# Kernel tuning notes

Hardware: AMD Instinct MI355X
Metric: run time of the kernel (lower is better)

The kernel has to match this reference:

```python
import jax, jax.numpy as jnp
import numpy as np

jax.config.update('jax_enable_x64', True)  # 60-bit packed voxel ids need int64

V, H, W, C, P = 8, 128, 128, 512, 128
VOXEL_SIZE = 0.05
NUM_VOXELS = 120000  # target_num_voxels; upper bound on unique voxels here
MAXI = (1 << 20) - 1


def _layernorm(x, g, b, eps=1e-5):
    mu = jnp.mean(x, axis=-1, keepdims=True)
    var = jnp.mean((x - mu) ** 2, axis=-1, keepdims=True)
    return (x - mu) * jax.lax.rsqrt(var + eps) * g + b


def setup_inputs() -> dict:
    key = jax.random.key(0)
    ks = jax.random.split(key, 16)
    features = jax.random.normal(ks[0], (V, H, W, C), jnp.float32)
    depth = jax.random.uniform(ks[1], (V, H, W), jnp.float32, minval=0.2, maxval=1.0)
    K = jnp.broadcast_to(jnp.array([[100.0, 0.0, W / 2.0], [0.0, 100.0, H / 2.0], [0.0, 0.0, 1.0]], jnp.float32), (V, 3, 3))
    R = jnp.broadcast_to(jnp.eye(3, dtype=jnp.float32), (V, 3, 3))
    t = jax.random.uniform(ks[2], (V, 3, 1), jnp.float32, minval=-0.1, maxval=0.1)
    extrinsics = jnp.concatenate([R, t], axis=-1)  # [V,3,4] world->cam
    conf = jax.random.normal(ks[3], (V, H, W), jnp.float32)
    s = 0.02
    return {
        'features': features, 'depth': depth, 'intrinsics': K, 'extrinsics': extrinsics, 'conf': conf,
        'w_proj1': jax.random.normal(ks[4], (C, C), jnp.float32) * s, 'b_proj1': jnp.zeros((C,), jnp.float32),
        'g_ln1': jnp.ones((C,), jnp.float32), 'be_ln1': jnp.zeros((C,), jnp.float32),
        'w_proj2': jax.random.normal(ks[5], (C, C), jnp.float32) * s, 'b_proj2': jnp.zeros((C,), jnp.float32),
        'w_pos1': jax.random.normal(ks[6], (3, P), jnp.float32) * s, 'b_pos1': jnp.zeros((P,), jnp.float32),
        'w_pos2': jax.random.normal(ks[7], (P, P), jnp.float32) * s, 'b_pos2': jnp.zeros((P,), jnp.float32),
        'w_fuse': jax.random.normal(ks[8], (C + P, C), jnp.float32) * s, 'b_fuse': jnp.zeros((C,), jnp.float32),
        'g_ln2': jnp.ones((C,), jnp.float32), 'be_ln2': jnp.zeros((C,), jnp.float32),
    }


def reference(features, depth, intrinsics, extrinsics, conf,
              w_proj1, b_proj1, g_ln1, be_ln1, w_proj2, b_proj2,
              w_pos1, b_pos1, w_pos2, b_pos2, w_fuse, b_fuse, g_ln2, be_ln2):
    # ---- backproject depth to world coords ----
    y, x = jnp.meshgrid(jnp.arange(H, dtype=depth.dtype), jnp.arange(W, dtype=depth.dtype), indexing='ij')
    pixels = jnp.stack([x, y, jnp.ones_like(x)], axis=-1).reshape(H * W, 3)  # [HW,3]
    Kinv = jnp.linalg.inv(intrinsics)                                        # [V,3,3]
    cam = jnp.einsum('vij,pj->vpi', Kinv, pixels) * depth.reshape(V, H * W, 1)
    cam_h = jnp.concatenate([cam, jnp.ones((V, H * W, 1), cam.dtype)], axis=-1)
    bottom = jnp.broadcast_to(jnp.array([[0.0, 0.0, 0.0, 1.0]], extrinsics.dtype), (V, 1, 4))
    E4 = jnp.concatenate([extrinsics, bottom], axis=1)                       # world->cam 4x4
    Einv = jnp.linalg.inv(E4)                                                # cam->world
    world = jnp.einsum('vij,vpj->vpi', Einv[:, :3, :], cam_h)                # [V,HW,3]
    pts = world.reshape(-1, 3)                                               # [N,3]

    # ---- voxel indices + packed 60-bit voxel id ----
    vox = pts / VOXEL_SIZE
    idx = jnp.round(vox).astype(jnp.int64)
    ix = jnp.clip(idx[:, 0], 0, MAXI)
    iy = jnp.clip(idx[:, 1], 0, MAXI)
    iz = jnp.clip(idx[:, 2], 0, MAXI)
    vid = (ix << 40) | (iy << 20) | iz                                       # [N]

    # ---- group points by voxel id (static-size unique -> segment ids) ----
    u_ids, seg = jnp.unique(vid, size=NUM_VOXELS, fill_value=-1, return_inverse=True)
    seg = seg.reshape(-1)

    # ---- per-voxel softmax pooling weights (scatter_max + scatter_add) ----
    scores = jax.nn.softplus(conf.reshape(-1))
    m = jax.ops.segment_max(scores, seg, num_segments=NUM_VOXELS)
    e = jnp.exp(scores - m[seg])
    denom = jax.ops.segment_sum(e, seg, num_segments=NUM_VOXELS)
    wgt = e / jnp.maximum(denom[seg], 1e-12)

    # ---- weighted scatter-add of features ----
    feats = features.reshape(-1, C)
    vfeat = jax.ops.segment_sum(feats * wgt[:, None], seg, num_segments=NUM_VOXELS)  # [S,C]

    # ---- voxel centers decoded from packed id ----
    cxi = (u_ids >> 40) & MAXI
    cyi = (u_ids >> 20) & MAXI
    czi = u_ids & MAXI
    valid = (u_ids >= 0)
    centers = jnp.stack([cxi, cyi, czi], axis=-1).astype(vfeat.dtype) * VOXEL_SIZE
    centers = jnp.where(valid[:, None], centers, 0.0)

    # ---- voxel_feat_proj: Linear -> LN -> GELU -> Linear ----
    h = vfeat @ w_proj1 + b_proj1
    h = jax.nn.gelu(_layernorm(h, g_ln1, be_ln1), approximate=False)
    h = h @ w_proj2 + b_proj2

    # ---- pos_encoding: Linear -> SiLU -> Linear ----
    pe = jax.nn.silu(centers @ w_pos1 + b_pos1) @ w_pos2 + b_pos2

    # ---- token_fusion: Linear -> LN -> GELU ----
    tok = jnp.concatenate([h, pe], axis=-1) @ w_fuse + b_fuse
    tok = jax.nn.gelu(_layernorm(tok, g_ln2, be_ln2), approximate=False)
    return tok * valid[:, None].astype(tok.dtype)
```

## Files before the change

kernel.cpp:

```cpp
#include <hip/hip_runtime.h>
#include <hip/hip_bf16.h>
#include <math.h>

#define V 8
#define H 128
#define W 128
#define C 512
#define P 128
#define HW (H*W)
#define NPTS (V*HW)
#define MAXI ((1<<20)-1)
#define ROWCAP 8192
#define NROWS 120000
#define DGRID 65536
#define PERM(d) ((((d) & 15) << 12) | ((d) >> 4))

#define SCAT_BLOCKS 512
#define WT_BLOCKS   832
#define POS_BLOCKS  (ROWCAP/8)
#define ZERO_BLOCKS 512
#define MEGA_BLOCKS (SCAT_BLOCKS + WT_BLOCKS + POS_BLOCKS + ZERO_BLOCKS)

typedef __attribute__((ext_vector_type(8))) short short8v;
typedef __attribute__((ext_vector_type(4))) float f32x4;

__device__ __forceinline__ float softplusf(float x){
  return fmaxf(x, 0.0f) + log1pf(expf(-fabsf(x)));
}
__device__ __forceinline__ float geluf(float x){
  return 0.5f * x * (1.0f + erff(x * 0.70710678118654752440f));
}
__device__ __forceinline__ short f2bf_s(float x){
  __hip_bfloat16 h = __float2bfloat16(x);
  return *(short*)&h;
}

__device__ void wT_tile(const float* __restrict__ w, __hip_bfloat16* __restrict__ wT,
                        int K, int bx, int by){
  __shared__ float tile[32][33];
  int kb = bx*32, nb = by*32;
  int tx = threadIdx.x & 31, ty = threadIdx.x >> 5;
  for (int i = ty; i < 32; i += 8){
    int k = kb + i;
    tile[i][tx] = (k < K) ? w[(size_t)k*512 + nb + tx] : 0.f;
  }
  __syncthreads();
  for (int i = ty; i < 32; i += 8){
    int n = nb + i;
    int k = kb + tx;
    if (k < K) wT[(size_t)n*K + k] = __float2bfloat16(tile[tx][i]);
  }
}

__global__ __launch_bounds__(256) void k_points(const float* __restrict__ depth,
    const float* __restrict__ Kmat, const float* __restrict__ Emat,
    int* __restrict__ scnt, unsigned short* __restrict__ didp, int* __restrict__ witp){
  int p = blockIdx.x*256 + threadIdx.x;
  int v = blockIdx.x >> 6;
  const float* K = Kmat + v*9;
  float a=K[0],b=K[1],c=K[2],d=K[3],e=K[4],f=K[5],g=K[6],h=K[7],i=K[8];
  float det = a*(e*i-f*h) - b*(d*i-f*g) + c*(d*h-e*g);
  float kin = 1.0f/det;
  float k0=(e*i-f*h)*kin, k1=(c*h-b*i)*kin, k2=(b*f-c*e)*kin;
  float k3=(f*g-d*i)*kin, k4=(a*i-c*g)*kin, k5=(c*d-a*f)*kin;
  float k6=(d*h-e*g)*kin, k7=(b*g-a*h)*kin, k8=(a*e-b*d)*kin;
  const float* E = Emat + v*12;
  float r00=E[0],r01=E[1],r02=E[2],t0=E[3];
  float r10=E[4],r11=E[5],r12=E[6],t1=E[7];
  float r20=E[8],r21=E[9],r22=E[10],t2=E[11];
  float rdet = r00*(r11*r22-r12*r21) - r01*(r10*r22-r12*r20) + r02*(r10*r21-r11*r20);
  float rinv = 1.0f/rdet;
  float i00=(r11*r22-r12*r21)*rinv, i01=(r02*r21-r01*r22)*rinv, i02=(r01*r12-r02*r11)*rinv;
  float i10=(r12*r20-r10*r22)*rinv, i11=(r00*r22-r02*r20)*rinv, i12=(r02*r10-r00*r12)*rinv;
  float i20=(r10*r21-r11*r20)*rinv, i21=(r01*r20-r00*r21)*rinv, i22=(r00*r11-r01*r10)*rinv;
  float j0=-(i00*t0+i01*t1+i02*t2), j1=-(i10*t0+i11*t1+i12*t2), j2=-(i20*t0+i21*t1+i22*t2);

  int pix = p & (HW-1);
  float fx = (float)(pix & 127);
  float fy = (float)(pix >> 7);
  float dep = depth[p];
  float cx = (k0*fx + k1*fy + k2) * dep;
  float cy = (k3*fx + k4*fy + k5) * dep;
  float cz = (k6*fx + k7*fy + k8) * dep;
  float wx = i00*cx + i01*cy + i02*cz + j0;
  float wy = i10*cx + i11*cy + i12*cz + j1;
  float wz = i20*cx + i21*cy + i22*cz + j2;
  long long ix = (long long)rintf(wx / 0.05f);
  long long iy = (long long)rintf(wy / 0.05f);
  long long iz = (long long)rintf(wz / 0.05f);
  ix = ix < 0 ? 0 : (ix > MAXI ? (long long)MAXI : ix);
  iy = iy < 0 ? 0 : (iy > MAXI ? (long long)MAXI : iy);
  iz = iz < 0 ? 0 : (iz > MAXI ? (long long)MAXI : iz);
  int dx = (int)(ix > 31 ? 31 : ix);
  int dy = (int)(iy > 31 ? 31 : iy);
  int dz = (int)(iz > 63 ? 63 : iz);
  int did = (dx << 11) | (dy << 6) | dz;
  didp[p] = (unsigned short)did;
  witp[p] = atomicAdd(&scnt[PERM(did)], 1);
}

__global__ __launch_bounds__(256) void k_scan1(const int* __restrict__ scnt,
    int* __restrict__ exwb, int* __restrict__ bsum){
  int tid = threadIdx.x;
  int did = blockIdx.x*256 + tid;
  int cnt = scnt[PERM(did)];
  int vpk = (cnt << 13) | (cnt > 0);
  int lane = tid & 63, wv = tid >> 6;
  int s = vpk;
  #pragma unroll
  for (int off = 1; off < 64; off <<= 1){
    int t = __shfl_up(s, off);
    if (lane >= off) s += t;
  }
  __shared__ int wsum[4];
  if (lane == 63) wsum[wv] = s;
  __syncthreads();
  int woff = 0;
  #pragma unroll
  for (int k = 0; k < 4; k++) woff += (k < wv) ? wsum[k] : 0;
  int incl = s + woff;
  exwb[did] = incl - vpk;
  if (tid == 255) bsum[blockIdx.x] = incl;
}

__global__ __launch_bounds__(256) void k_scan2(const int* __restrict__ scnt,
    const int* __restrict__ exwb, const int* __restrict__ bsum,
    int* __restrict__ row_of_dense, int* __restrict__ ustart_dense,
    int* __restrict__ dense_of_row, int* __restrict__ Sc){
  int tid = threadIdx.x, b = blockIdx.x;
  int lane = tid & 63, wv = tid >> 6;
  int vsum = (tid < b) ? bsum[tid] : 0;
  #pragma unroll
  for (int off = 32; off; off >>= 1) vsum += __shfl_down(vsum, off);
  __shared__ int rsum[4];
  if (lane == 0) rsum[wv] = vsum;
  __syncthreads();
  int prefix = rsum[0] + rsum[1] + rsum[2] + rsum[3];
  int did = b*256 + tid;
  int cnt = scnt[PERM(did)];
  int excl = exwb[did] + prefix;
  ustart_dense[did] = excl >> 13;
  int row = excl & 8191;
  row_of_dense[did] = row;
  if (cnt > 0) dense_of_row[row] = did;
  if (b == 255 && tid == 255)
    *Sc = (excl + ((cnt << 13) | (cnt > 0))) & 8191;
}

__global__ __launch_bounds__(256) void k_fill(const unsigned short* __restrict__ didp,
    const int* __restrict__ witp, const int* __restrict__ row_of_dense,
    const int* __restrict__ ustart_dense, const float* __restrict__ conf,
    int* __restrict__ pcsr, int* __restrict__ rcsr, float* __restrict__ wcsr){
  int p = blockIdx.x*256 + threadIdx.x;
  int did = didp[p];
  int idx = ustart_dense[did] + witp[p];
  pcsr[idx] = p;
  rcsr[idx] = row_of_dense[did];
  wcsr[idx] = expf(softplusf(conf[p]));
}

__global__ __launch_bounds__(256) void k_mega(
    const float* __restrict__ feats,
    const int* __restrict__ pcsr, const int* __restrict__ rcsr, const float* __restrict__ wcsr,
    float* __restrict__ vraw, float* __restrict__ esum,
    float* __restrict__ outp, const int* __restrict__ Sc,
    const int* __restrict__ dense_of_row,
    const float* __restrict__ wp1, const float* __restrict__ bp1,
    const float* __restrict__ wp2, const float* __restrict__ bp2,
    __hip_bfloat16* __restrict__ pebf,
    const float* __restrict__ w1, __hip_bfloat16* __restrict__ w1T,
    const float* __restrict__ w2, __hip_bfloat16* __restrict__ w2T,
    const float* __restrict__ wf, __hip_bfloat16* __restrict__ wfT){
  int blk = blockIdx.x;
  int tid = threadIdx.x;

  if (blk < SCAT_BLOCKS){
    __shared__ int pp[4][64];
    __shared__ int rr[4][64];
    __shared__ float ww[4][64];
    int q = tid >> 6, ln = tid & 63;
    int e = blk*256 + q*64 + ln;
    pp[q][ln] = pcsr[e];
    rr[q][ln] = rcsr[e];
    ww[q][ln] = wcsr[e];
    __syncthreads();
    f32x4 acc0 = (f32x4){0.f,0.f,0.f,0.f};
    f32x4 acc1 = (f32x4){0.f,0.f,0.f,0.f};
    float acce = 0.f;
    int cur = rr[q][0];
    #define FLUSH_ROW() { \
      float* vp = &vraw[(size_t)cur*C + ln*4]; \
      atomicAdd(vp+0, acc0[0]); atomicAdd(vp+1, acc0[1]); \
      atomicAdd(vp+2, acc0[2]); atomicAdd(vp+3, acc0[3]); \
      float* vq = vp + 256; \
      atomicAdd(vq+0, acc1[0]); atomicAdd(vq+1, acc1[1]); \
      atomicAdd(vq+2, acc1[2]); atomicAdd(vq+3, acc1[3]); \
      if (ln == 0) atomicAdd(&esum[cur], acce); \
      acc0 = (f32x4){0.f,0.f,0.f,0.f}; acc1 = (f32x4){0.f,0.f,0.f,0.f}; acce = 0.f; }
    for (int i = 0; i < 64; i += 4){
      int p0 = pp[q][i+0], p1 = pp[q][i+1], p2 = pp[q][i+2], p3 = pp[q][i+3];
      const float* f0 = feats + (size_t)p0*C + ln*4;
      const float* f1 = feats + (size_t)p1*C + ln*4;
      const float* f2 = feats + (size_t)p2*C + ln*4;
      const float* f3 = feats + (size_t)p3*C + ln*4;
      f32x4 a0 = *(const f32x4*)f0, b0 = *(const f32x4*)(f0 + 256);
      f32x4 a1 = *(const f32x4*)f1, b1 = *(const f32x4*)(f1 + 256);
      f32x4 a2 = *(const f32x4*)f2, b2 = *(const f32x4*)(f2 + 256);
      f32x4 a3 = *(const f32x4*)f3, b3 = *(const f32x4*)(f3 + 256);
      int r0 = rr[q][i+0], r1 = rr[q][i+1], r2 = rr[q][i+2], r3 = rr[q][i+3];
      float w0 = ww[q][i+0], w1_ = ww[q][i+1], w2_ = ww[q][i+2], w3 = ww[q][i+3];
      if (r0 != cur){ FLUSH_ROW(); cur = r0; }
      acc0 += a0 * w0; acc1 += b0 * w0; acce += w0;
      if (r1 != cur){ FLUSH_ROW(); cur = r1; }
      acc0 += a1 * w1_; acc1 += b1 * w1_; acce += w1_;
      if (r2 != cur){ FLUSH_ROW(); cur = r2; }
      acc0 += a2 * w2_; acc1 += b2 * w2_; acce += w2_;
      if (r3 != cur){ FLUSH_ROW(); cur = r3; }
      acc0 += a3 * w3; acc1 += b3 * w3; acce += w3;
    }
    FLUSH_ROW();
    #undef FLUSH_ROW
    return;
  }
  blk -= SCAT_BLOCKS;

  if (blk < WT_BLOCKS){
    if (blk < 256)      wT_tile(w1, w1T, 512, blk & 15, blk >> 4);
    else if (blk < 512){ int t = blk - 256; wT_tile(w2, w2T, 512, t & 15, t >> 4); }
    else               { int t = blk - 512; wT_tile(wf, wfT, 640, t % 20, t / 20); }
    return;
  }
  blk -= WT_BLOCKS;

  if (blk < POS_BLOCKS){
    int S = *Sc; if (S > ROWCAP) S = ROWCAP;
    int r0 = blk * 8;
    if (r0 >= S) return;
    __shared__ float t1[8][128];
    __shared__ float cen[8][4];
    if (tid < 8){
      int r = r0 + tid;
      int d = (r < S) ? dense_of_row[r] : 0;
      cen[tid][0] = (float)(d >> 11) * 0.05f;
      cen[tid][1] = (float)((d >> 6) & 31) * 0.05f;
      cen[tid][2] = (float)(d & 63) * 0.05f;
    }
    __syncthreads();
    #pragma unroll
    for (int it = 0; it < 4; it++){
      int idx = tid + it*256;
      int r = idx >> 7, j = idx & 127;
      float a = cen[r][0]*wp1[j] + cen[r][1]*wp1[P + j] + cen[r][2]*wp1[2*P + j] + bp1[j];
      t1[r][j] = a / (1.0f + expf(-a));
    }
    __syncthreads();
    #pragma unroll
    for (int it = 0; it < 4; it++){
      int idx = tid + it*256;
      int r = idx >> 7, j = idx & 127;
      if (r0 + r < S){
        float acc = bp2[j];
        for (int k = 0; k < P; k++) acc = fmaf(t1[r][k], wp2[k*P + j], acc);
        pebf[(size_t)(r0+r)*P + j] = __float2bfloat16(acc);
      }
    }
    return;
  }
  blk -= POS_BLOCKS;

  {
    int S = *Sc; if (S > ROWCAP) S = ROWCAP;
    f32x4* out4 = (f32x4*)outp;
    size_t start = (size_t)S * 128;
    size_t total = (size_t)NROWS * 128;
    size_t stride = (size_t)ZERO_BLOCKS * 256;
    f32x4 z = (f32x4){0.f,0.f,0.f,0.f};
    for (size_t idx = start + (size_t)blk*256 + tid; idx < total; idx += stride)
      __builtin_nontemporal_store(z, &out4[idx]);
  }
}

__global__ __launch_bounds__(256) void k_gemm1(const float* __restrict__ vraw,
    const float* __restrict__ esum, const __hip_bfloat16* __restrict__ Bt,
    const float* __restrict__ bias, float* __restrict__ Cout, const int* __restrict__ Sc){
  int S = *Sc; if (S > ROWCAP) S = ROWCAP;
  int m0 = blockIdx.y * 64;
  if (m0 >= S) return;
  int n0 = blockIdx.x * 64;
  __shared__ short As[64][40];
  __shared__ short Bs[64][40];
  int tid = threadIdx.x;
  int l = tid & 63, w = tid >> 6;
  int wr = w >> 1, wc = w & 1;
  f32x4 acc[2][2];
  #pragma unroll
  for (int i=0;i<2;i++)
    #pragma unroll
    for (int j=0;j<2;j++) acc[i][j] = (f32x4){0.f,0.f,0.f,0.f};

  int arow = tid >> 2, akq = tid & 3;
  int gm = m0 + arow;
  float inv = 0.f;
  if (gm < S) inv = 1.0f / fmaxf(esum[gm], 1e-12f);
  for (int kb = 0; kb < 512; kb += 32){
    {
      int kg = kb + akq*8;
      short8v av = (short8v){0,0,0,0,0,0,0,0};
      if (gm < S){
        f32x4 va = *(const f32x4*)(vraw + (size_t)gm*512 + kg);
        f32x4 vb = *(const f32x4*)(vraw + (size_t)gm*512 + kg + 4);
        av[0]=f2bf_s(va[0]*inv); av[1]=f2bf_s(va[1]*inv);
        av[2]=f2bf_s(va[2]*inv); av[3]=f2bf_s(va[3]*inv);
        av[4]=f2bf_s(vb[0]*inv); av[5]=f2bf_s(vb[1]*inv);
        av[6]=f2bf_s(vb[2]*inv); av[7]=f2bf_s(vb[3]*inv);
      }
      *(short8v*)&As[arow][akq*8] = av;
      short8v bv = *(const short8v*)(Bt + (size_t)(n0 + arow)*512 + kb + akq*8);
      *(short8v*)&Bs[arow][akq*8] = bv;
    }
    __syncthreads();
    short8v a0 = *(const short8v*)&As[wr*32 + (l & 15)][(l >> 4)*8];
    short8v a1 = *(const short8v*)&As[wr*32 + 16 + (l & 15)][(l >> 4)*8];
    short8v b0 = *(const short8v*)&Bs[wc*32 + (l & 15)][(l >> 4)*8];
    short8v b1 = *(const short8v*)&Bs[wc*32 + 16 + (l & 15)][(l >> 4)*8];
    acc[0][0] = __builtin_amdgcn_mfma_f32_16x16x32_bf16(a0, b0, acc[0][0], 0, 0, 0);
    acc[0][1] = __builtin_amdgcn_mfma_f32_16x16x32_bf16(a0, b1, acc[0][1], 0, 0, 0);
    acc[1][0] = __builtin_amdgcn_mfma_f32_16x16x32_bf16(a1, b0, acc[1][0], 0, 0, 0);
    acc[1][1] = __builtin_amdgcn_mfma_f32_16x16x32_bf16(a1, b1, acc[1][1], 0, 0, 0);
    __syncthreads();
  }
  float bias0 = bias[n0 + wc*32 +  0 + (l & 15)];
  float bias1 = bias[n0 + wc*32 + 16 + (l & 15)];
  #pragma unroll
  for (int i = 0; i < 2; i++){
    #pragma unroll
    for (int j = 0; j < 2; j++){
      int n = n0 + wc*32 + j*16 + (l & 15);
      float bj = j ? bias1 : bias0;
      #pragma unroll
      for (int r = 0; r < 4; r++){
        int m = m0 + wr*32 + i*16 + (l >> 4)*4 + r;
        if (m < S) Cout[(size_t)m*512 + n] = acc[i][j][r] + bj;
      }
    }
  }
}

template<int OUTBF>
__global__ __launch_bounds__(256) void k_gemm_mfma(
    const __hip_bfloat16* __restrict__ A1, int lda1, int K1,
    const __hip_bfloat16* __restrict__ A2, int lda2,
    const __hip_bfloat16* __restrict__ Bt, int ldb,
    const float* __restrict__ bias, void* __restrict__ Cout,
    int Kdim, const int* __restrict__ Sc){
  int S = *Sc; if (S > ROWCAP) S = ROWCAP;
  int m0 = blockIdx.y * 64;
  if (m0 >= S) return;
  int n0 = blockIdx.x * 64;
  __shared__ short As[64][40];
  __shared__ short Bs[64][40];
  int tid = threadIdx.x;
  int l = tid & 63, w = tid >> 6;
  int wr = w >> 1, wc = w & 1;
  f32x4 acc[2][2];
  #pragma unroll
  for (int i=0;i<2;i++)
    #pragma unroll
    for (int j=0;j<2;j++) acc[i][j] = (f32x4){0.f,0.f,0.f,0.f};

  int arow = tid >> 2, akq = tid & 3;
  for (int kb = 0; kb < Kdim; kb += 32){
    {
      int kg = kb + akq*8;
      short8v av = (short8v){0,0,0,0,0,0,0,0};
      int gm = m0 + arow;
      if (gm < S){
        const __hip_bfloat16* src = (kg < K1) ? (A1 + (size_t)gm*lda1 + kg)
                                              : (A2 + (size_t)gm*lda2 + (kg - K1));
        av = *(const short8v*)src;
      }
      *(short8v*)&As[arow][akq*8] = av;
      short8v bv = *(const short8v*)(Bt + (size_t)(n0 + arow)*ldb + kb + akq*8);
      *(short8v*)&Bs[arow][akq*8] = bv;
    }
    __syncthreads();
    short8v a0 = *(const short8v*)&As[wr*32 + (l & 15)][(l >> 4)*8];
    short8v a1 = *(const short8v*)&As[wr*32 + 16 + (l & 15)][(l >> 4)*8];
    short8v b0 = *(const short8v*)&Bs[wc*32 + (l & 15)][(l >> 4)*8];
    short8v b1 = *(const short8v*)&Bs[wc*32 + 16 + (l & 15)][(l >> 4)*8];
    acc[0][0] = __builtin_amdgcn_mfma_f32_16x16x32_bf16(a0, b0, acc[0][0], 0, 0, 0);
    acc[0][1] = __builtin_amdgcn_mfma_f32_16x16x32_bf16(a0, b1, acc[0][1], 0, 0, 0);
    acc[1][0] = __builtin_amdgcn_mfma_f32_16x16x32_bf16(a1, b0, acc[1][0], 0, 0, 0);
    acc[1][1] = __builtin_amdgcn_mfma_f32_16x16x32_bf16(a1, b1, acc[1][1], 0, 0, 0);
    __syncthreads();
  }
  float bias0 = bias[n0 + wc*32 +  0 + (l & 15)];
  float bias1 = bias[n0 + wc*32 + 16 + (l & 15)];
  #pragma unroll
  for (int i = 0; i < 2; i++){
    #pragma unroll
    for (int j = 0; j < 2; j++){
      int n = n0 + wc*32 + j*16 + (l & 15);
      float bj = j ? bias1 : bias0;
      #pragma unroll
      for (int r = 0; r < 4; r++){
        int m = m0 + wr*32 + i*16 + (l >> 4)*4 + r;
        if (m < S){
          float val = acc[i][j][r] + bj;
          if (OUTBF) ((__hip_bfloat16*)Cout)[(size_t)m*512 + n] = __float2bfloat16(val);
          else       ((float*)Cout)[(size_t)m*512 + n] = val;
        }
      }
    }
  }
}

__global__ __launch_bounds__(256) void k_ln_gelu(const float* __restrict__ in,
    __hip_bfloat16* __restrict__ outp, const float* __restrict__ g, const float* __restrict__ b,
    const int* __restrict__ Sc){
  int S = *Sc; if (S > ROWCAP) S = ROWCAP;
  __shared__ float red[8];
  int lane = threadIdx.x & 63, wid = threadIdx.x >> 6;
  for (int row = blockIdx.x; row < S; row += gridDim.x){
    float x0 = in[(size_t)row*C + threadIdx.x];
    float x1 = in[(size_t)row*C + threadIdx.x + 256];
    float s = x0 + x1;
    for (int o_=32;o_;o_>>=1) s += __shfl_down(s, o_);
    if (lane == 0) red[wid] = s;
    __syncthreads();
    float mu = (red[0]+red[1]+red[2]+red[3]) * (1.0f/C);
    __syncthreads();
    float d0 = x0-mu, d1 = x1-mu;
    float q = d0*d0 + d1*d1;
    for (int o_=32;o_;o_>>=1) q += __shfl_down(q, o_);
    if (lane == 0) red[wid] = q;
    __syncthreads();
    float var = (red[0]+red[1]+red[2]+red[3]) * (1.0f/C);
    float rs = rsqrtf(var + 1e-5f);
    float y0 = d0*rs*g[threadIdx.x]     + b[threadIdx.x];
    float y1 = d1*rs*g[threadIdx.x+256] + b[threadIdx.x+256];
    outp[(size_t)row*C + threadIdx.x]       = __float2bfloat16(geluf(y0));
    outp[(size_t)row*C + threadIdx.x + 256] = __float2bfloat16(geluf(y1));
    __syncthreads();
  }
}

__global__ __launch_bounds__(256) void k_ln_gelu_out(const float* __restrict__ in,
    float* __restrict__ outp, const float* __restrict__ g, const float* __restrict__ b,
    const int* __restrict__ Sc){
  int S = *Sc; if (S > ROWCAP) S = ROWCAP;
  __shared__ float red[8];
  int lane = threadIdx.x & 63, wid = threadIdx.x >> 6;
  for (int row = blockIdx.x; row < S; row += gridDim.x){
    float x0 = in[(size_t)row*C + threadIdx.x];
    float x1 = in[(size_t)row*C + threadIdx.x + 256];
    float s = x0 + x1;
    for (int o_=32;o_;o_>>=1) s += __shfl_down(s, o_);
    if (lane == 0) red[wid] = s;
    __syncthreads();
    float mu = (red[0]+red[1]+red[2]+red[3]) * (1.0f/C);
    __syncthreads();
    float d0 = x0-mu, d1 = x1-mu;
    float q = d0*d0 + d1*d1;
    for (int o_=32;o_;o_>>=1) q += __shfl_down(q, o_);
    if (lane == 0) red[wid] = q;
    __syncthreads();
    float var = (red[0]+red[1]+red[2]+red[3]) * (1.0f/C);
    float rs = rsqrtf(var + 1e-5f);
    float y0 = d0*rs*g[threadIdx.x]     + b[threadIdx.x];
    float y1 = d1*rs*g[threadIdx.x+256] + b[threadIdx.x+256];
    __builtin_nontemporal_store(geluf(y0), &outp[(size_t)row*C + threadIdx.x]);
    __builtin_nontemporal_store(geluf(y1), &outp[(size_t)row*C + threadIdx.x + 256]);
    __syncthreads();
  }
}

extern "C" void kernel_launch(void* const* d_in, const int* in_sizes, int n_in,
                              void* d_out, int out_size, void* d_ws, size_t ws_size,
                              hipStream_t stream){
  const float* features = (const float*)d_in[0];
  const float* depth    = (const float*)d_in[1];
  const float* intr     = (const float*)d_in[2];
  const float* extr     = (const float*)d_in[3];
  const float* conf     = (const float*)d_in[4];
  const float* w1  = (const float*)d_in[5];
  const float* b1  = (const float*)d_in[6];
  const float* g1  = (const float*)d_in[7];
  const float* be1 = (const float*)d_in[8];
  const float* w2  = (const float*)d_in[9];
  const float* b2  = (const float*)d_in[10];
  const float* wp1 = (const float*)d_in[11];
  const float* bp1 = (const float*)d_in[12];
  const float* wp2 = (const float*)d_in[13];
  const float* bp2 = (const float*)d_in[14];
  const float* wf  = (const float*)d_in[15];
  const float* bf  = (const float*)d_in[16];
  const float* g2  = (const float*)d_in[17];
  const float* be2 = (const float*)d_in[18];

  char* ws = (char*)d_ws;
  size_t o = 0;
  auto alloc = [&](size_t bytes){ void* p = ws + o; o += (bytes + 255) & ~size_t(255); return p; };
  int*   scnt    = (int*)alloc((size_t)DGRID*4);
  int*   Sc      = (int*)alloc(256);
  float* esum    = (float*)alloc((size_t)ROWCAP*4);
  float* vraw    = (float*)alloc((size_t)ROWCAP*C*4);
  size_t zspan = (size_t)((char*)vraw + (size_t)ROWCAP*C*4 - (char*)scnt);
  unsigned short* didp = (unsigned short*)alloc((size_t)NPTS*2);
  int*   witp    = (int*)alloc((size_t)NPTS*4);
  int*   pcsr    = (int*)alloc((size_t)NPTS*4);
  int*   rcsr    = (int*)alloc((size_t)NPTS*4);
  float* wcsr    = (float*)alloc((size_t)NPTS*4);
  int*   exwb    = (int*)alloc((size_t)DGRID*4);
  int*   bsum    = (int*)alloc(256*4);
  int*   row_of_dense   = (int*)alloc((size_t)DGRID*4);
  int*   ustart_dense   = (int*)alloc((size_t)DGRID*4);
  int*   dense_of_row   = (int*)alloc((size_t)ROWCAP*4);
  float*          hbufA = (float*)alloc((size_t)ROWCAP*C*4);
  __hip_bfloat16* h1bf = (__hip_bfloat16*)alloc((size_t)ROWCAP*C*2);
  __hip_bfloat16* h2bf = (__hip_bfloat16*)alloc((size_t)ROWCAP*C*2);
  __hip_bfloat16* pebf = (__hip_bfloat16*)alloc((size_t)ROWCAP*P*2);
  __hip_bfloat16* w1T  = (__hip_bfloat16*)alloc((size_t)512*512*2);
  __hip_bfloat16* w2T  = (__hip_bfloat16*)alloc((size_t)512*512*2);
  __hip_bfloat16* wfT  = (__hip_bfloat16*)alloc((size_t)512*640*2);

  float* outp = (float*)d_out;

  hipMemsetAsync(scnt, 0, zspan, stream);

  k_points<<<NPTS/256, 256, 0, stream>>>(depth, intr, extr, scnt, didp, witp);
  k_scan1<<<DGRID/256, 256, 0, stream>>>(scnt, exwb, bsum);
  k_scan2<<<DGRID/256, 256, 0, stream>>>(scnt, exwb, bsum, row_of_dense, ustart_dense,
                                         dense_of_row, Sc);
  k_fill<<<NPTS/256, 256, 0, stream>>>(didp, witp, row_of_dense, ustart_dense, conf,
                                       pcsr, rcsr, wcsr);
  k_mega<<<MEGA_BLOCKS, 256, 0, stream>>>(features, pcsr, rcsr, wcsr, vraw, esum,
                                          outp, Sc, dense_of_row,
                                          wp1, bp1, wp2, bp2, pebf,
                                          w1, w1T, w2, w2T, wf, wfT);

  dim3 gg(512/64, ROWCAP/64);
  k_gemm1<<<gg, 256, 0, stream>>>(vraw, esum, w1T, b1, hbufA, Sc);
  k_ln_gelu<<<2048, 256, 0, stream>>>(hbufA, h1bf, g1, be1, Sc);
  k_gemm_mfma<1><<<gg, 256, 0, stream>>>(h1bf, 512, 512, h1bf, 512, w2T, 512, b2, h2bf, 512, Sc);
  k_gemm_mfma<0><<<gg, 256, 0, stream>>>(h2bf, 512, 512, pebf, 128, wfT, 640, bf, hbufA, 640, Sc);
  k_ln_gelu_out<<<2048, 256, 0, stream>>>(hbufA, outp, g2, be2, Sc);
}
```

Baseline: 233.9 us.

## Spread output tail zero-fill across earlier kernels and widen scatter ILP

```diff
diff --git a/kernel.cpp b/kernel.cpp
--- a/kernel.cpp
+++ b/kernel.cpp
@@ -11,15 +11,19 @@
 #define NPTS (V*HW)
 #define MAXI ((1<<20)-1)
 #define ROWCAP 8192
+#define PROWCAP 5376
 #define NROWS 120000
 #define DGRID 65536
 #define PERM(d) ((((d) & 15) << 12) | ((d) >> 4))
-
-#define SCAT_BLOCKS 512
+#define NCH 5
+
+#define SCAT_BLOCKS 1024
 #define WT_BLOCKS   832
 #define POS_BLOCKS  (ROWCAP/8)
-#define ZERO_BLOCKS 512
-#define MEGA_BLOCKS (SCAT_BLOCKS + WT_BLOCKS + POS_BLOCKS + ZERO_BLOCKS)
+#define MEGA_BLOCKS (SCAT_BLOCKS + WT_BLOCKS + POS_BLOCKS)
+
+#define PZB 512
+#define GZB 512
 
 typedef __attribute__((ext_vector_type(8))) short short8v;
 typedef __attribute__((ext_vector_type(4))) float f32x4;
@@ -33,6 +37,21 @@
 __device__ __forceinline__ short f2bf_s(float x){
   __hip_bfloat16 h = __float2bfloat16(x);
   return *(short*)&h;
+}
+
+__device__ __forceinline__ void zero_chunk(float* __restrict__ outp, int chunk,
+                                           int nblocks, int blk, int tid){
+  f32x4* out4 = (f32x4*)outp;
+  size_t start = (size_t)PROWCAP * 128;
+  size_t total = (size_t)NROWS * 128;
+  size_t n = total - start;
+  size_t per = (n + NCH - 1) / NCH;
+  size_t cs = start + (size_t)chunk * per;
+  size_t ce = cs + per; if (ce > total) ce = total;
+  size_t stride = (size_t)nblocks * 256;
+  f32x4 z = (f32x4){0.f,0.f,0.f,0.f};
+  for (size_t i = cs + (size_t)blk*256 + tid; i < ce; i += stride)
+    __builtin_nontemporal_store(z, &out4[i]);
 }
 
 __device__ void wT_tile(const float* __restrict__ w, __hip_bfloat16* __restrict__ wT,
@@ -54,9 +73,13 @@
 
 __global__ __launch_bounds__(256) void k_points(const float* __restrict__ depth,
     const float* __restrict__ Kmat, const float* __restrict__ Emat,
-    int* __restrict__ scnt, unsigned short* __restrict__ didp, int* __restrict__ witp){
-  int p = blockIdx.x*256 + threadIdx.x;
-  int v = blockIdx.x >> 6;
+    int* __restrict__ scnt, unsigned short* __restrict__ didp, int* __restrict__ witp,
+    float* __restrict__ outp){
+  int blk = blockIdx.x;
+  int tid = threadIdx.x;
+  if (blk >= NPTS/256){ zero_chunk(outp, 0, PZB, blk - NPTS/256, tid); return; }
+  int p = blk*256 + tid;
+  int v = blk >> 6;
   const float* K = Kmat + v*9;
   float a=K[0],b=K[1],c=K[2],d=K[3],e=K[4],f=K[5],g=K[6],h=K[7],i=K[8];
   float det = a*(e*i-f*h) - b*(d*i-f*g) + c*(d*h-e*g);
@@ -163,8 +186,7 @@
     const float* __restrict__ feats,
     const int* __restrict__ pcsr, const int* __restrict__ rcsr, const float* __restrict__ wcsr,
     float* __restrict__ vraw, float* __restrict__ esum,
-    float* __restrict__ outp, const int* __restrict__ Sc,
-    const int* __restrict__ dense_of_row,
+    const int* __restrict__ Sc, const int* __restrict__ dense_of_row,
     const float* __restrict__ wp1, const float* __restrict__ bp1,
     const float* __restrict__ wp2, const float* __restrict__ bp2,
     __hip_bfloat16* __restrict__ pebf,
@@ -175,15 +197,17 @@
   int tid = threadIdx.x;
 
   if (blk < SCAT_BLOCKS){
-    __shared__ int pp[4][64];
-    __shared__ int rr[4][64];
-    __shared__ float ww[4][64];
+    __shared__ int pp[4][32];
+    __shared__ int rr[4][32];
+    __shared__ float ww[4][32];
+    if (tid < 128){
+      int e = blk*128 + tid;
+      pp[tid>>5][tid&31] = pcsr[e];
+      rr[tid>>5][tid&31] = rcsr[e];
+      ww[tid>>5][tid&31] = wcsr[e];
+    }
+    __syncthreads();
     int q = tid >> 6, ln = tid & 63;
-    int e = blk*256 + q*64 + ln;
-    pp[q][ln] = pcsr[e];
-    rr[q][ln] = rcsr[e];
-    ww[q][ln] = wcsr[e];
-    __syncthreads();
     f32x4 acc0 = (f32x4){0.f,0.f,0.f,0.f};
     f32x4 acc1 = (f32x4){0.f,0.f,0.f,0.f};
     float acce = 0.f;
@@ -197,26 +221,33 @@
       atomicAdd(vq+2, acc1[2]); atomicAdd(vq+3, acc1[3]); \
       if (ln == 0) atomicAdd(&esum[cur], acce); \
       acc0 = (f32x4){0.f,0.f,0.f,0.f}; acc1 = (f32x4){0.f,0.f,0.f,0.f}; acce = 0.f; }
-    for (int i = 0; i < 64; i += 4){
-      int p0 = pp[q][i+0], p1 = pp[q][i+1], p2 = pp[q][i+2], p3 = pp[q][i+3];
-      const float* f0 = feats + (size_t)p0*C + ln*4;
-      const float* f1 = feats + (size_t)p1*C + ln*4;
-      const float* f2 = feats + (size_t)p2*C + ln*4;
-      const float* f3 = feats + (size_t)p3*C + ln*4;
-      f32x4 a0 = *(const f32x4*)f0, b0 = *(const f32x4*)(f0 + 256);
-      f32x4 a1 = *(const f32x4*)f1, b1 = *(const f32x4*)(f1 + 256);
-      f32x4 a2 = *(const f32x4*)f2, b2 = *(const f32x4*)(f2 + 256);
-      f32x4 a3 = *(const f32x4*)f3, b3 = *(const f32x4*)(f3 + 256);
-      int r0 = rr[q][i+0], r1 = rr[q][i+1], r2 = rr[q][i+2], r3 = rr[q][i+3];
-      float w0 = ww[q][i+0], w1_ = ww[q][i+1], w2_ = ww[q][i+2], w3 = ww[q][i+3];
-      if (r0 != cur){ FLUSH_ROW(); cur = r0; }
-      acc0 += a0 * w0; acc1 += b0 * w0; acce += w0;
-      if (r1 != cur){ FLUSH_ROW(); cur = r1; }
-      acc0 += a1 * w1_; acc1 += b1 * w1_; acce += w1_;
-      if (r2 != cur){ FLUSH_ROW(); cur = r2; }
-      acc0 += a2 * w2_; acc1 += b2 * w2_; acce += w2_;
-      if (r3 != cur){ FLUSH_ROW(); cur = r3; }
-      acc0 += a3 * w3; acc1 += b3 * w3; acce += w3;
+    for (int i = 0; i < 32; i += 8){
+      f32x4 a0,a1,a2,a3,a4,a5,a6,a7, b0,b1,b2,b3,b4,b5,b6,b7;
+      {
+        const float* f0 = feats + (size_t)pp[q][i+0]*C + ln*4;
+        const float* f1 = feats + (size_t)pp[q][i+1]*C + ln*4;
+        const float* f2 = feats + (size_t)pp[q][i+2]*C + ln*4;
+        const float* f3 = feats + (size_t)pp[q][i+3]*C + ln*4;
+        const float* f4 = feats + (size_t)pp[q][i+4]*C + ln*4;
+        const float* f5 = feats + (size_t)pp[q][i+5]*C + ln*4;
+        const float* f6 = feats + (size_t)pp[q][i+6]*C + ln*4;
+        const float* f7 = feats + (size_t)pp[q][i+7]*C + ln*4;
+        a0 = *(const f32x4*)f0; b0 = *(const f32x4*)(f0 + 256);
+        a1 = *(const f32x4*)f1; b1 = *(const f32x4*)(f1 + 256);
+        a2 = *(const f32x4*)f2; b2 = *(const f32x4*)(f2 + 256);
+        a3 = *(const f32x4*)f3; b3 = *(const f32x4*)(f3 + 256);
+        a4 = *(const f32x4*)f4; b4 = *(const f32x4*)(f4 + 256);
+        a5 = *(const f32x4*)f5; b5 = *(const f32x4*)(f5 + 256);
+        a6 = *(const f32x4*)f6; b6 = *(const f32x4*)(f6 + 256);
+        a7 = *(const f32x4*)f7; b7 = *(const f32x4*)(f7 + 256);
+      }
+      #define STEP(u, av, bv) { \
+        int r_ = rr[q][i+u]; float w_ = ww[q][i+u]; \
+        if (r_ != cur){ FLUSH_ROW(); cur = r_; } \
+        acc0 += av * w_; acc1 += bv * w_; acce += w_; }
+      STEP(0, a0, b0) STEP(1, a1, b1) STEP(2, a2, b2) STEP(3, a3, b3)
+      STEP(4, a4, b4) STEP(5, a5, b5) STEP(6, a6, b6) STEP(7, a7, b7)
+      #undef STEP
     }
     FLUSH_ROW();
     #undef FLUSH_ROW
@@ -232,7 +263,7 @@
   }
   blk -= WT_BLOCKS;
 
-  if (blk < POS_BLOCKS){
+  {
     int S = *Sc; if (S > ROWCAP) S = ROWCAP;
     int r0 = blk * 8;
     if (r0 >= S) return;
@@ -264,32 +295,22 @@
         pebf[(size_t)(r0+r)*P + j] = __float2bfloat16(acc);
       }
     }
-    return;
-  }
-  blk -= POS_BLOCKS;
-
-  {
-    int S = *Sc; if (S > ROWCAP) S = ROWCAP;
-    f32x4* out4 = (f32x4*)outp;
-    size_t start = (size_t)S * 128;
-    size_t total = (size_t)NROWS * 128;
-    size_t stride = (size_t)ZERO_BLOCKS * 256;
-    f32x4 z = (f32x4){0.f,0.f,0.f,0.f};
-    for (size_t idx = start + (size_t)blk*256 + tid; idx < total; idx += stride)
-      __builtin_nontemporal_store(z, &out4[idx]);
   }
 }
 
 __global__ __launch_bounds__(256) void k_gemm1(const float* __restrict__ vraw,
     const float* __restrict__ esum, const __hip_bfloat16* __restrict__ Bt,
-    const float* __restrict__ bias, float* __restrict__ Cout, const int* __restrict__ Sc){
+    const float* __restrict__ bias, float* __restrict__ Cout, const int* __restrict__ Sc,
+    float* __restrict__ outz){
+  int blk = blockIdx.x;
+  int tid = threadIdx.x;
+  if (blk >= 1024){ zero_chunk(outz, 1, GZB, blk - 1024, tid); return; }
   int S = *Sc; if (S > ROWCAP) S = ROWCAP;
-  int m0 = blockIdx.y * 64;
+  int m0 = (blk >> 3) * 64;
   if (m0 >= S) return;
-  int n0 = blockIdx.x * 64;
+  int n0 = (blk & 7) * 64;
   __shared__ short As[64][40];
   __shared__ short Bs[64][40];
-  int tid = threadIdx.x;
   int l = tid & 63, w = tid >> 6;
   int wr = w >> 1, wc = w & 1;
   f32x4 acc[2][2];
@@ -346,20 +367,22 @@
   }
 }
 
-template<int OUTBF>
+template<int OUTBF, int CHUNK>
 __global__ __launch_bounds__(256) void k_gemm_mfma(
     const __hip_bfloat16* __restrict__ A1, int lda1, int K1,
     const __hip_bfloat16* __restrict__ A2, int lda2,
     const __hip_bfloat16* __restrict__ Bt, int ldb,
     const float* __restrict__ bias, void* __restrict__ Cout,
-    int Kdim, const int* __restrict__ Sc){
+    int Kdim, const int* __restrict__ Sc, float* __restrict__ outz){
+  int blk = blockIdx.x;
+  int tid = threadIdx.x;
+  if (blk >= 1024){ zero_chunk(outz, CHUNK, GZB, blk - 1024, tid); return; }
   int S = *Sc; if (S > ROWCAP) S = ROWCAP;
-  int m0 = blockIdx.y * 64;
+  int m0 = (blk >> 3) * 64;
   if (m0 >= S) return;
-  int n0 = blockIdx.x * 64;
+  int n0 = (blk & 7) * 64;
   __shared__ short As[64][40];
   __shared__ short Bs[64][40];
-  int tid = threadIdx.x;
   int l = tid & 63, w = tid >> 6;
   int wr = w >> 1, wc = w & 1;
   f32x4 acc[2][2];
@@ -417,13 +440,15 @@
 
 __global__ __launch_bounds__(256) void k_ln_gelu(const float* __restrict__ in,
     __hip_bfloat16* __restrict__ outp, const float* __restrict__ g, const float* __restrict__ b,
-    const int* __restrict__ Sc){
+    const int* __restrict__ Sc, float* __restrict__ outz){
+  int tid = threadIdx.x;
+  if (blockIdx.x >= 2048){ zero_chunk(outz, 2, GZB, blockIdx.x - 2048, tid); return; }
   int S = *Sc; if (S > ROWCAP) S = ROWCAP;
   __shared__ float red[8];
-  int lane = threadIdx.x & 63, wid = threadIdx.x >> 6;
-  for (int row = blockIdx.x; row < S; row += gridDim.x){
-    float x0 = in[(size_t)row*C + threadIdx.x];
-    float x1 = in[(size_t)row*C + threadIdx.x + 256];
+  int lane = tid & 63, wid = tid >> 6;
+  for (int row = blockIdx.x; row < S; row += 2048){
+    float x0 = in[(size_t)row*C + tid];
+    float x1 = in[(size_t)row*C + tid + 256];
     float s = x0 + x1;
     for (int o_=32;o_;o_>>=1) s += __shfl_down(s, o_);
     if (lane == 0) red[wid] = s;
@@ -437,10 +462,10 @@
     __syncthreads();
     float var = (red[0]+red[1]+red[2]+red[3]) * (1.0f/C);
     float rs = rsqrtf(var + 1e-5f);
-    float y0 = d0*rs*g[threadIdx.x]     + b[threadIdx.x];
-    float y1 = d1*rs*g[threadIdx.x+256] + b[threadIdx.x+256];
-    outp[(size_t)row*C + threadIdx.x]       = __float2bfloat16(geluf(y0));
-    outp[(size_t)row*C + threadIdx.x + 256] = __float2bfloat16(geluf(y1));
+    float y0 = d0*rs*g[tid]     + b[tid];
+    float y1 = d1*rs*g[tid+256] + b[tid+256];
+    outp[(size_t)row*C + tid]       = __float2bfloat16(geluf(y0));
+    outp[(size_t)row*C + tid + 256] = __float2bfloat16(geluf(y1));
     __syncthreads();
   }
 }
@@ -450,10 +475,11 @@
     const int* __restrict__ Sc){
   int S = *Sc; if (S > ROWCAP) S = ROWCAP;
   __shared__ float red[8];
-  int lane = threadIdx.x & 63, wid = threadIdx.x >> 6;
+  int tid = threadIdx.x;
+  int lane = tid & 63, wid = tid >> 6;
   for (int row = blockIdx.x; row < S; row += gridDim.x){
-    float x0 = in[(size_t)row*C + threadIdx.x];
-    float x1 = in[(size_t)row*C + threadIdx.x + 256];
+    float x0 = in[(size_t)row*C + tid];
+    float x1 = in[(size_t)row*C + tid + 256];
     float s = x0 + x1;
     for (int o_=32;o_;o_>>=1) s += __shfl_down(s, o_);
     if (lane == 0) red[wid] = s;
@@ -467,11 +493,15 @@
     __syncthreads();
     float var = (red[0]+red[1]+red[2]+red[3]) * (1.0f/C);
     float rs = rsqrtf(var + 1e-5f);
-    float y0 = d0*rs*g[threadIdx.x]     + b[threadIdx.x];
-    float y1 = d1*rs*g[threadIdx.x+256] + b[threadIdx.x+256];
-    __builtin_nontemporal_store(geluf(y0), &outp[(size_t)row*C + threadIdx.x]);
-    __builtin_nontemporal_store(geluf(y1), &outp[(size_t)row*C + threadIdx.x + 256]);
-    __syncthreads();
+    float y0 = d0*rs*g[tid]     + b[tid];
+    float y1 = d1*rs*g[tid+256] + b[tid+256];
+    __builtin_nontemporal_store(geluf(y0), &outp[(size_t)row*C + tid]);
+    __builtin_nontemporal_store(geluf(y1), &outp[(size_t)row*C + tid + 256]);
+    __syncthreads();
+  }
+  for (int row = S + blockIdx.x; row < PROWCAP; row += gridDim.x){
+    __builtin_nontemporal_store(0.f, &outp[(size_t)row*C + tid]);
+    __builtin_nontemporal_store(0.f, &outp[(size_t)row*C + tid + 256]);
   }
 }
 
@@ -528,21 +558,22 @@
 
   hipMemsetAsync(scnt, 0, zspan, stream);
 
-  k_points<<<NPTS/256, 256, 0, stream>>>(depth, intr, extr, scnt, didp, witp);
+  k_points<<<NPTS/256 + PZB, 256, 0, stream>>>(depth, intr, extr, scnt, didp, witp, outp);
   k_scan1<<<DGRID/256, 256, 0, stream>>>(scnt, exwb, bsum);
   k_scan2<<<DGRID/256, 256, 0, stream>>>(scnt, exwb, bsum, row_of_dense, ustart_dense,
                                          dense_of_row, Sc);
   k_fill<<<NPTS/256, 256, 0, stream>>>(didp, witp, row_of_dense, ustart_dense, conf,
                                        pcsr, rcsr, wcsr);
   k_mega<<<MEGA_BLOCKS, 256, 0, stream>>>(features, pcsr, rcsr, wcsr, vraw, esum,
-                                          outp, Sc, dense_of_row,
+                                          Sc, dense_of_row,
                                           wp1, bp1, wp2, bp2, pebf,
                                           w1, w1T, w2, w2T, wf, wfT);
 
-  dim3 gg(512/64, ROWCAP/64);
-  k_gemm1<<<gg, 256, 0, stream>>>(vraw, esum, w1T, b1, hbufA, Sc);
-  k_ln_gelu<<<2048, 256, 0, stream>>>(hbufA, h1bf, g1, be1, Sc);
-  k_gemm_mfma<1><<<gg, 256, 0, stream>>>(h1bf, 512, 512, h1bf, 512, w2T, 512, b2, h2bf, 512, Sc);
-  k_gemm_mfma<0><<<gg, 256, 0, stream>>>(h2bf, 512, 512, pebf, 128, wfT, 640, bf, hbufA, 640, Sc);
+  k_gemm1<<<1024 + GZB, 256, 0, stream>>>(vraw, esum, w1T, b1, hbufA, Sc, outp);
+  k_ln_gelu<<<2048 + GZB, 256, 0, stream>>>(hbufA, h1bf, g1, be1, Sc, outp);
+  k_gemm_mfma<1,3><<<1024 + GZB, 256, 0, stream>>>(h1bf, 512, 512, h1bf, 512, w2T, 512,
+                                                   b2, h2bf, 512, Sc, outp);
+  k_gemm_mfma<0,4><<<1024 + GZB, 256, 0, stream>>>(h2bf, 512, 512, pebf, 128, wfT, 640,
+                                                   bf, hbufA, 640, Sc, outp);
   k_ln_gelu_out<<<2048, 256, 0, stream>>>(hbufA, outp, g2, be2, Sc);
 }
```

New measurement: 237.8 us. No clear change (+1.7%).
